# Performance work log

Measured on AMD Instinct MI355X. Metric: run time of the kernel, lower is better.

The kernel has to match this reference:

```python
import jax, jax.numpy as jnp
import numpy as np

K_NEIGHBOURS = 40  # includes self; self is dropped after top-k


def setup_inputs() -> dict:
    key = jax.random.key(0)
    ks = jax.random.split(key, 4)
    B, V, F_in = 4, 4096, 64
    P, S, F_out = 64, 4, 64
    x = jax.random.normal(ks[0], (B, V, F_in), dtype=jnp.float32)
    Wf = jax.random.normal(ks[1], (F_in, P), dtype=jnp.float32) / np.sqrt(F_in)
    bf = jnp.zeros((P,), dtype=jnp.float32)
    Ws = jax.random.normal(ks[2], (F_in, S), dtype=jnp.float32) / np.sqrt(F_in)
    bs = jnp.zeros((S,), dtype=jnp.float32)
    Wo = jax.random.normal(ks[3], (F_in + 2 * P, F_out), dtype=jnp.float32) / np.sqrt(F_in + 2 * P)
    bo = jnpp = jnp.zeros((F_out,), dtype=jnp.float32)
    return {"x": x, "Wf": Wf, "bf": bf, "Ws": Ws, "bs": bs, "Wo": Wo, "bo": bo}


def _euclidean_squared(c):
    # c: [B, V, S] -> [B, V, V] squared pairwise distances
    sq = jnp.sum(c * c, axis=-1)  # [B, V]
    d2 = sq[:, :, None] + sq[:, None, :] - 2.0 * jnp.einsum('bvs,bus->bvu', c, c)
    return d2


def reference(x, Wf, bf, Ws, bs, Wo, bo):
    # learned spatial coordinates and propagated features
    coords = x @ Ws + bs            # [B, V, S]
    feats = x @ Wf + bf             # [B, V, P]

    d2 = _euclidean_squared(coords)                 # [B, V, V]
    neg_vals, idx = jax.lax.top_k(-d2, K_NEIGHBOURS)  # closest first (self at 0)
    nbr_idx = idx[:, :, 1:]                         # [B, V, K-1]
    dist = -neg_vals[:, :, 1:]                      # [B, V, K-1] (>= 0)

    # gauss_of_lin(d * 10) = exp(-|10 d|)
    w = jnp.exp(-jnp.abs(dist * 10.0))              # [B, V, K-1]

    # gather neighbour features per batch: [B, V, K-1, P]
    nf = jax.vmap(lambda f, i: f[i])(feats, nbr_idx)
    nf = nf * w[..., None]

    collected = jnp.concatenate([jnp.max(nf, axis=2), jnp.mean(nf, axis=2)], axis=-1)  # [B, V, 2P]
    updated = jnp.concatenate([x, collected], axis=-1)  # [B, V, F_in + 2P]
    return jnp.tanh(updated @ Wo + bo)
```

## Files before the change

### kernel.cpp

```cpp
#include <hip/hip_runtime.h>
#include <cmath>

#define BB  4
#define VV  4096
#define KK  40
#define FIN 64

typedef float v2f __attribute__((ext_vector_type(2)));

__global__ __launch_bounds__(256) void prep_kernel(
    const float* __restrict__ x, const float* __restrict__ Wf,
    const float* __restrict__ bf, const float* __restrict__ Ws,
    const float* __restrict__ bs,
    float* __restrict__ coords, float* __restrict__ sq,
    float* __restrict__ feats)
{
    int lane = threadIdx.x & 63;
    int wid  = threadIdx.x >> 6;
    int row0 = (blockIdx.x * 4 + wid) * 4;
    const float* xr = x + (size_t)row0 * FIN;

    float a0 = 0.f, a1 = 0.f, a2 = 0.f, a3 = 0.f;
    #pragma unroll 8
    for (int k = 0; k < FIN; ++k) {
        float wf = Wf[k * 64 + lane];
        a0 = fmaf(xr[k],        wf, a0);
        a1 = fmaf(xr[64  + k],  wf, a1);
        a2 = fmaf(xr[128 + k],  wf, a2);
        a3 = fmaf(xr[192 + k],  wf, a3);
    }
    float bfl = bf[lane];
    feats[(size_t)(row0 + 0) * 64 + lane] = a0 + bfl;
    feats[(size_t)(row0 + 1) * 64 + lane] = a1 + bfl;
    feats[(size_t)(row0 + 2) * 64 + lane] = a2 + bfl;
    feats[(size_t)(row0 + 3) * 64 + lane] = a3 + bfl;

    int r  = lane >> 4;
    int s  = (lane >> 2) & 3;
    int kc = lane & 3;
    const float* xrr = x + (size_t)(row0 + r) * FIN + kc * 16;
    const float* wsr = Ws + kc * 16 * 4 + s;
    float c = 0.f;
    #pragma unroll
    for (int k = 0; k < 16; ++k)
        c = fmaf(xrr[k], wsr[k * 4], c);
    c += __shfl_xor(c, 1, 64);
    c += __shfl_xor(c, 2, 64);
    float val = c + bs[s];
    if ((lane & 3) == 0) coords[(size_t)(row0 + r) * 4 + s] = val;
    float p = val * val;
    p += __shfl_xor(p, 4, 64);
    p += __shfl_xor(p, 8, 64);
    if ((lane & 15) == 0) sq[row0 + r] = p;
}

__global__ __launch_bounds__(256) void gravnet_kernel(
    const float* __restrict__ x, const float* __restrict__ coords,
    const float* __restrict__ sq, const float* __restrict__ feats,
    const float* __restrict__ Wo, const float* __restrict__ bo,
    float* __restrict__ out)
{
    int lane = threadIdx.x & 63;
    int wid  = threadIdx.x >> 6;
    int q0   = (blockIdx.x * 4 + wid) * 4;
    int b    = q0 >> 12;
    int v0   = q0 & (VV - 1);

    __shared__ uint2               s_nb[4][4][KK];
    __shared__ __align__(16) float s_upd[4][4][192];

    const float4* cb  = (const float4*)(coords + (size_t)b * VV * 4);
    const float*  sqb = sq + (size_t)b * VV;

    v2f nx[2], ny[2], nz[2], nw[2], hs[2];
    #pragma unroll
    for (int p = 0; p < 2; ++p) {
        float4 cqa = cb[v0 + 2 * p];
        float4 cqb = cb[v0 + 2 * p + 1];
        nx[p] = (v2f){-2.f * cqa.x, -2.f * cqb.x};
        ny[p] = (v2f){-2.f * cqa.y, -2.f * cqb.y};
        nz[p] = (v2f){-2.f * cqa.z, -2.f * cqb.z};
        nw[p] = (v2f){-2.f * cqa.w, -2.f * cqb.w};
        hs[p] = (v2f){sqb[v0 + 2 * p], sqb[v0 + 2 * p + 1]};
    }

    unsigned mm[4][4];
    #pragma unroll
    for (int qq = 0; qq < 4; ++qq)
        mm[qq][0] = mm[qq][1] = mm[qq][2] = mm[qq][3] = 0xFFFFFFFFu;

    #pragma unroll 4
    for (int i = 0; i < 64; ++i) {
        int u = i * 64 + lane;
        float4 cu  = cb[u];
        float  squ = sqb[u];
        float d2s[4];
        #pragma unroll
        for (int p = 0; p < 2; ++p) {
            v2f acc = hs[p] + (v2f){squ, squ};
            acc = __builtin_elementwise_fma(nx[p], (v2f){cu.x, cu.x}, acc);
            acc = __builtin_elementwise_fma(ny[p], (v2f){cu.y, cu.y}, acc);
            acc = __builtin_elementwise_fma(nz[p], (v2f){cu.z, cu.z}, acc);
            acc = __builtin_elementwise_fma(nw[p], (v2f){cu.w, cu.w}, acc);
            d2s[2 * p]     = acc.x;
            d2s[2 * p + 1] = acc.y;
        }
        #pragma unroll
        for (int qq = 0; qq < 4; ++qq) {
            float d2 = fmaxf(d2s[qq], 0.f);
            unsigned key = (__float_as_uint(d2) & 0xFFFFF000u) | (unsigned)u;
            unsigned b0 = max(mm[qq][0], key);
            unsigned b1 = max(mm[qq][1], key);
            unsigned b2 = max(mm[qq][2], key);
            mm[qq][0] = min(mm[qq][0], key);
            mm[qq][1] = min(mm[qq][1], b0);
            mm[qq][2] = min(mm[qq][2], b1);
            mm[qq][3] = min(mm[qq][3], b2);
        }
    }

    unsigned M[4] = {0u, 0u, 0u, 0u};
    for (int bit = 30; bit >= 0; --bit) {
        #pragma unroll
        for (int qq = 0; qq < 4; ++qq) {
            unsigned cand = M[qq] | (1u << bit);
            int cnt = (int)__popcll(__ballot(mm[qq][0] < cand))
                    + (int)__popcll(__ballot(mm[qq][1] < cand))
                    + (int)__popcll(__ballot(mm[qq][2] < cand))
                    + (int)__popcll(__ballot(mm[qq][3] < cand));
            if (cnt <= 39) M[qq] = cand;
        }
    }

    #pragma unroll
    for (int qq = 0; qq < 4; ++qq) {
        unsigned mn = mm[qq][0];
        #pragma unroll
        for (int off = 32; off >= 1; off >>= 1) {
            unsigned o = __shfl_xor(mn, off, 64);
            mn = o < mn ? o : mn;
        }
        int base = 0;
        #pragma unroll
        for (int i = 0; i < 4; ++i) {
            unsigned kk = mm[qq][i];
            bool pred = (kk <= M[qq]) && (kk != mn);
            unsigned long long mask = __ballot(pred);
            unsigned pos = (unsigned)base +
                __builtin_amdgcn_mbcnt_hi((unsigned)(mask >> 32),
                    __builtin_amdgcn_mbcnt_lo((unsigned)mask, 0u));
            if (pred) {
                float d2a = __uint_as_float(kk & 0xFFFFF000u);
                float w   = __expf(-10.f * d2a);
                s_nb[wid][qq][pos] =
                    make_uint2((kk & 4095u) << 8, __float_as_uint(w));
            }
            base += (int)__popcll(mask);
        }
    }

    const float* fb  = feats + (size_t)b * VV * 64;
    const char*  fbl = (const char*)(fb + lane);
    float vmax[4], vsum[4];
    #pragma unroll
    for (int qq = 0; qq < 4; ++qq) { vmax[qq] = -INFINITY; vsum[qq] = 0.f; }
    #pragma unroll 3
    for (int j = 0; j < KK - 1; ++j) {
        #pragma unroll
        for (int qq = 0; qq < 4; ++qq) {
            uint2 nb = s_nb[wid][qq][j];
            float f  = *(const float*)(fbl + nb.x);
            float w  = __uint_as_float(nb.y);
            float val = w * f;
            vmax[qq] = fmaxf(vmax[qq], val);
            vsum[qq] += val;
        }
    }

    #pragma unroll
    for (int qq = 0; qq < 4; ++qq) {
        s_upd[wid][qq][lane]       = x[(size_t)(q0 + qq) * 64 + lane];
        s_upd[wid][qq][64  + lane] = vmax[qq];
        s_upd[wid][qq][128 + lane] = vsum[qq] * (1.0f / 39.0f);
    }

    float bol = bo[lane];
    float acc[4] = { bol, bol, bol, bol };
    #pragma unroll 4
    for (int j4 = 0; j4 < 48; ++j4) {
        float wo0 = Wo[(j4 * 4 + 0) * 64 + lane];
        float wo1 = Wo[(j4 * 4 + 1) * 64 + lane];
        float wo2 = Wo[(j4 * 4 + 2) * 64 + lane];
        float wo3 = Wo[(j4 * 4 + 3) * 64 + lane];
        #pragma unroll
        for (int qq = 0; qq < 4; ++qq) {
            float4 uv = *(const float4*)&s_upd[wid][qq][j4 * 4];
            acc[qq] = fmaf(uv.x, wo0, acc[qq]);
            acc[qq] = fmaf(uv.y, wo1, acc[qq]);
            acc[qq] = fmaf(uv.z, wo2, acc[qq]);
            acc[qq] = fmaf(uv.w, wo3, acc[qq]);
        }
    }
    #pragma unroll
    for (int qq = 0; qq < 4; ++qq) {
        float e = __expf(2.f * acc[qq]);
        out[(size_t)(q0 + qq) * 64 + lane] = 1.f - __fdividef(2.f, e + 1.f);
    }
}

extern "C" void kernel_launch(void* const* d_in, const int* in_sizes, int n_in,
                              void* d_out, int out_size, void* d_ws, size_t ws_size,
                              hipStream_t stream)
{
    (void)in_sizes; (void)n_in; (void)out_size; (void)ws_size;
    const float* x  = (const float*)d_in[0];
    const float* Wf = (const float*)d_in[1];
    const float* bf = (const float*)d_in[2];
    const float* Ws = (const float*)d_in[3];
    const float* bs = (const float*)d_in[4];
    const float* Wo = (const float*)d_in[5];
    const float* bo = (const float*)d_in[6];
    float* out = (float*)d_out;

    float* coords = (float*)d_ws;
    float* sq     = coords + (size_t)BB * VV * 4;
    float* feats  = sq + (size_t)BB * VV;

    prep_kernel<<<BB * VV / 16, 256, 0, stream>>>(x, Wf, bf, Ws, bs,
                                                  coords, sq, feats);
    gravnet_kernel<<<BB * VV / 16, 256, 0, stream>>>(x, coords, sq, feats,
                                                     Wo, bo, out);
}
```

Baseline: 132.9 us.

## Halve queries per wave to double wave count and recompute squared norms inline

```diff
diff --git a/kernel.cpp b/kernel.cpp
--- a/kernel.cpp
+++ b/kernel.cpp
@@ -54,7 +54,7 @@
     if ((lane & 15) == 0) sq[row0 + r] = p;
 }
 
-__global__ __launch_bounds__(256) void gravnet_kernel(
+__global__ __launch_bounds__(256, 8) void gravnet_kernel(
     const float* __restrict__ x, const float* __restrict__ coords,
     const float* __restrict__ sq, const float* __restrict__ feats,
     const float* __restrict__ Wo, const float* __restrict__ bo,
@@ -62,51 +62,44 @@
 {
     int lane = threadIdx.x & 63;
     int wid  = threadIdx.x >> 6;
-    int q0   = (blockIdx.x * 4 + wid) * 4;
+    int q0   = (blockIdx.x * 4 + wid) * 2;
     int b    = q0 >> 12;
     int v0   = q0 & (VV - 1);
 
-    __shared__ uint2               s_nb[4][4][KK];
-    __shared__ __align__(16) float s_upd[4][4][192];
+    __shared__ uint2               s_nb[4][2][KK];
+    __shared__ __align__(16) float s_upd[4][2][192];
 
     const float4* cb  = (const float4*)(coords + (size_t)b * VV * 4);
     const float*  sqb = sq + (size_t)b * VV;
 
-    v2f nx[2], ny[2], nz[2], nw[2], hs[2];
-    #pragma unroll
-    for (int p = 0; p < 2; ++p) {
-        float4 cqa = cb[v0 + 2 * p];
-        float4 cqb = cb[v0 + 2 * p + 1];
-        nx[p] = (v2f){-2.f * cqa.x, -2.f * cqb.x};
-        ny[p] = (v2f){-2.f * cqa.y, -2.f * cqb.y};
-        nz[p] = (v2f){-2.f * cqa.z, -2.f * cqb.z};
-        nw[p] = (v2f){-2.f * cqa.w, -2.f * cqb.w};
-        hs[p] = (v2f){sqb[v0 + 2 * p], sqb[v0 + 2 * p + 1]};
-    }
-
-    unsigned mm[4][4];
-    #pragma unroll
-    for (int qq = 0; qq < 4; ++qq)
+    float4 cqa = cb[v0], cqb = cb[v0 + 1];
+    v2f nx = (v2f){-2.f * cqa.x, -2.f * cqb.x};
+    v2f ny = (v2f){-2.f * cqa.y, -2.f * cqb.y};
+    v2f nz = (v2f){-2.f * cqa.z, -2.f * cqb.z};
+    v2f nw = (v2f){-2.f * cqa.w, -2.f * cqb.w};
+    v2f hs = (v2f){sqb[v0], sqb[v0 + 1]};
+
+    unsigned mm[2][4];
+    #pragma unroll
+    for (int qq = 0; qq < 2; ++qq)
         mm[qq][0] = mm[qq][1] = mm[qq][2] = mm[qq][3] = 0xFFFFFFFFu;
 
     #pragma unroll 4
     for (int i = 0; i < 64; ++i) {
         int u = i * 64 + lane;
-        float4 cu  = cb[u];
-        float  squ = sqb[u];
-        float d2s[4];
-        #pragma unroll
-        for (int p = 0; p < 2; ++p) {
-            v2f acc = hs[p] + (v2f){squ, squ};
-            acc = __builtin_elementwise_fma(nx[p], (v2f){cu.x, cu.x}, acc);
-            acc = __builtin_elementwise_fma(ny[p], (v2f){cu.y, cu.y}, acc);
-            acc = __builtin_elementwise_fma(nz[p], (v2f){cu.z, cu.z}, acc);
-            acc = __builtin_elementwise_fma(nw[p], (v2f){cu.w, cu.w}, acc);
-            d2s[2 * p]     = acc.x;
-            d2s[2 * p + 1] = acc.y;
-        }
-        #pragma unroll
-        for (int qq = 0; qq < 4; ++qq) {
+        float4 cu = cb[u];
+        float squ = cu.x * cu.x;
+        squ = fmaf(cu.y, cu.y, squ);
+        squ = fmaf(cu.z, cu.z, squ);
+        squ = fmaf(cu.w, cu.w, squ);
+        v2f acc = hs + (v2f){squ, squ};
+        acc = __builtin_elementwise_fma(nx, (v2f){cu.x, cu.x}, acc);
+        acc = __builtin_elementwise_fma(ny, (v2f){cu.y, cu.y}, acc);
+        acc = __builtin_elementwise_fma(nz, (v2f){cu.z, cu.z}, acc);
+        acc = __builtin_elementwise_fma(nw, (v2f){cu.w, cu.w}, acc);
+        float d2s[2] = { acc.x, acc.y };
+        #pragma unroll
+        for (int qq = 0; qq < 2; ++qq) {
             float d2 = fmaxf(d2s[qq], 0.f);
             unsigned key = (__float_as_uint(d2) & 0xFFFFF000u) | (unsigned)u;
             unsigned b0 = max(mm[qq][0], key);
@@ -119,10 +112,10 @@
         }
     }
 
-    unsigned M[4] = {0u, 0u, 0u, 0u};
+    unsigned M[2] = {0u, 0u};
     for (int bit = 30; bit >= 0; --bit) {
         #pragma unroll
-        for (int qq = 0; qq < 4; ++qq) {
+        for (int qq = 0; qq < 2; ++qq) {
             unsigned cand = M[qq] | (1u << bit);
             int cnt = (int)__popcll(__ballot(mm[qq][0] < cand))
                     + (int)__popcll(__ballot(mm[qq][1] < cand))
@@ -133,7 +126,7 @@
     }
 
     #pragma unroll
-    for (int qq = 0; qq < 4; ++qq) {
+    for (int qq = 0; qq < 2; ++qq) {
         unsigned mn = mm[qq][0];
         #pragma unroll
         for (int off = 32; off >= 1; off >>= 1) {
@@ -161,13 +154,13 @@
 
     const float* fb  = feats + (size_t)b * VV * 64;
     const char*  fbl = (const char*)(fb + lane);
-    float vmax[4], vsum[4];
-    #pragma unroll
-    for (int qq = 0; qq < 4; ++qq) { vmax[qq] = -INFINITY; vsum[qq] = 0.f; }
-    #pragma unroll 3
+    float vmax[2], vsum[2];
+    #pragma unroll
+    for (int qq = 0; qq < 2; ++qq) { vmax[qq] = -INFINITY; vsum[qq] = 0.f; }
+    #pragma unroll 6
     for (int j = 0; j < KK - 1; ++j) {
         #pragma unroll
-        for (int qq = 0; qq < 4; ++qq) {
+        for (int qq = 0; qq < 2; ++qq) {
             uint2 nb = s_nb[wid][qq][j];
             float f  = *(const float*)(fbl + nb.x);
             float w  = __uint_as_float(nb.y);
@@ -178,34 +171,31 @@
     }
 
     #pragma unroll
-    for (int qq = 0; qq < 4; ++qq) {
+    for (int qq = 0; qq < 2; ++qq) {
         s_upd[wid][qq][lane]       = x[(size_t)(q0 + qq) * 64 + lane];
         s_upd[wid][qq][64  + lane] = vmax[qq];
         s_upd[wid][qq][128 + lane] = vsum[qq] * (1.0f / 39.0f);
     }
 
     float bol = bo[lane];
-    float acc[4] = { bol, bol, bol, bol };
+    float acc0 = bol, acc1 = bol;
     #pragma unroll 4
     for (int j4 = 0; j4 < 48; ++j4) {
         float wo0 = Wo[(j4 * 4 + 0) * 64 + lane];
         float wo1 = Wo[(j4 * 4 + 1) * 64 + lane];
         float wo2 = Wo[(j4 * 4 + 2) * 64 + lane];
         float wo3 = Wo[(j4 * 4 + 3) * 64 + lane];
-        #pragma unroll
-        for (int qq = 0; qq < 4; ++qq) {
-            float4 uv = *(const float4*)&s_upd[wid][qq][j4 * 4];
-            acc[qq] = fmaf(uv.x, wo0, acc[qq]);
-            acc[qq] = fmaf(uv.y, wo1, acc[qq]);
-            acc[qq] = fmaf(uv.z, wo2, acc[qq]);
-            acc[qq] = fmaf(uv.w, wo3, acc[qq]);
-        }
-    }
-    #pragma unroll
-    for (int qq = 0; qq < 4; ++qq) {
-        float e = __expf(2.f * acc[qq]);
-        out[(size_t)(q0 + qq) * 64 + lane] = 1.f - __fdividef(2.f, e + 1.f);
-    }
+        float4 u0 = *(const float4*)&s_upd[wid][0][j4 * 4];
+        float4 u1 = *(const float4*)&s_upd[wid][1][j4 * 4];
+        acc0 = fmaf(u0.x, wo0, acc0);  acc1 = fmaf(u1.x, wo0, acc1);
+        acc0 = fmaf(u0.y, wo1, acc0);  acc1 = fmaf(u1.y, wo1, acc1);
+        acc0 = fmaf(u0.z, wo2, acc0);  acc1 = fmaf(u1.z, wo2, acc1);
+        acc0 = fmaf(u0.w, wo3, acc0);  acc1 = fmaf(u1.w, wo3, acc1);
+    }
+    float e0 = __expf(2.f * acc0);
+    float e1 = __expf(2.f * acc1);
+    out[(size_t)q0 * 64 + lane]       = 1.f - __fdividef(2.f, e0 + 1.f);
+    out[(size_t)(q0 + 1) * 64 + lane] = 1.f - __fdividef(2.f, e1 + 1.f);
 }
 
 extern "C" void kernel_launch(void* const* d_in, const int* in_sizes, int n_in,
@@ -228,6 +218,6 @@
 
     prep_kernel<<<BB * VV / 16, 256, 0, stream>>>(x, Wf, bf, Ws, bs,
                                                   coords, sq, feats);
-    gravnet_kernel<<<BB * VV / 16, 256, 0, stream>>>(x, coords, sq, feats,
-                                                     Wo, bo, out);
+    gravnet_kernel<<<BB * VV / 8, 256, 0, stream>>>(x, coords, sq, feats,
+                                                    Wo, bo, out);
 }
```

After: 133.1 us. About the same (+0.2%).
